# Performance work log

Hardware: AMD Instinct MI355X
Metric: run time of the kernel (lower is better)

Reference implementation:

```python
import jax, jax.numpy as jnp
import numpy as np

T = 0.07  # softmax temperature from __init__
N_QUEUES = 4


def _l2norm(x, axis):
    return x / jnp.maximum(jnp.linalg.norm(x, axis=axis, keepdims=True), 1e-12)


def setup_inputs() -> dict:
    key = jax.random.key(0)
    k1, k2, k3, k4, k5, k6 = jax.random.split(key, 6)
    N, D_in, dim, K = 512, 2048, 128, 65536
    im_q = jax.random.normal(k1, (N, D_in), dtype=jnp.float32)
    im_k = jax.random.normal(k2, (N, D_in), dtype=jnp.float32)
    W_q = jax.random.normal(k3, (D_in, dim), dtype=jnp.float32) * (1.0 / np.sqrt(D_in))
    W_k = jax.random.normal(k4, (D_in, dim), dtype=jnp.float32) * (1.0 / np.sqrt(D_in))
    queues = jax.random.normal(k5, (N_QUEUES, dim, K), dtype=jnp.float32)
    queues = _l2norm(queues, axis=1)  # normalize along feature dim, as in __init__
    label = jax.random.randint(k6, (N,), 0, 4, dtype=jnp.int32)
    return {"im_q": im_q, "im_k": im_k, "W_q": W_q, "W_k": W_k,
            "queues": queues, "label": label}


def reference(im_q, im_k, W_q, W_k, queues, label):
    # encoder_q / encoder_k abstracted as linear projections
    q = _l2norm(im_q @ W_q, axis=1)                      # [N, C]
    k = _l2norm(im_k @ W_k, axis=1)                      # [N, C] (no_grad in original)
    l_pos = jnp.einsum('nc,nc->n', q, k)[:, None]        # [N, 1]
    # per-sample queue routing: queue index = (label - 1) % 4
    route = jnp.mod(label - 1, N_QUEUES)                 # [N]
    onehot = jax.nn.one_hot(route, N_QUEUES, dtype=q.dtype)  # [N, G]
    # l_neg[n, k] = sum_c q[n, c] * queues[route[n], c, k], as grouped matmul
    l_neg = jnp.einsum('ngc,gck->nk', q[:, None, :] * onehot[:, :, None], queues)  # [N, K]
    logits = jnp.concatenate([l_pos, l_neg], axis=1) / T  # [N, 1+K]
    labels = jnp.zeros(logits.shape[0], dtype=jnp.int32)
    return logits, labels
```

## Files before the change

kernel.cpp:

```cpp
#include <hip/hip_runtime.h>

typedef short short8 __attribute__((ext_vector_type(8)));
typedef float floatx4 __attribute__((ext_vector_type(4)));

__device__ __forceinline__ unsigned short f2bf(float f) {
  unsigned u = __float_as_uint(f);
  u += 0x7FFFu + ((u >> 16) & 1u);
  return (unsigned short)(u >> 16);
}

__global__ __launch_bounds__(256) void proj_partial(
    const float* __restrict__ im_q, const float* __restrict__ im_k,
    const float* __restrict__ Wq, const float* __restrict__ Wk,
    float* __restrict__ part, int* __restrict__ cnt) {
  __shared__ float imS[32 * 260];
  const int t = threadIdx.x;
  if (blockIdx.x == 0 && blockIdx.y == 0 && blockIdx.z == 0 && t < 4) cnt[t] = 0;
  const int which = blockIdx.z;
  const float* __restrict__ im = which ? im_k : im_q;
  const float* __restrict__ W  = which ? Wk : Wq;
  const int d0 = blockIdx.x * 256;
  const int row0 = blockIdx.y * 32;
  {
    const int dd0 = (t & 63) * 4;
    const int rb = t >> 6;
#pragma unroll
    for (int p = 0; p < 8; ++p) {
      const int r = rb + p * 4;
      const float4 v = *(const float4*)(im + (size_t)(row0 + r) * 2048 + d0 + dd0);
      *(float4*)(imS + r * 260 + dd0) = v;
    }
  }
  __syncthreads();
  const int c4 = (t & 31) * 4;
  const int r4 = (t >> 5) * 4;
  float acc[4][4] = {};
  const float* __restrict__ Wp = W + (size_t)d0 * 128 + c4;
#pragma unroll 4
  for (int d = 0; d < 256; ++d) {
    const float4 w = *(const float4*)(Wp + (size_t)d * 128);
    float a[4];
#pragma unroll
    for (int rr = 0; rr < 4; ++rr) a[rr] = imS[(r4 + rr) * 260 + d];
#pragma unroll
    for (int rr = 0; rr < 4; ++rr) {
      acc[rr][0] += a[rr] * w.x;
      acc[rr][1] += a[rr] * w.y;
      acc[rr][2] += a[rr] * w.z;
      acc[rr][3] += a[rr] * w.w;
    }
  }
#pragma unroll
  for (int rr = 0; rr < 4; ++rr) {
    float4 v = make_float4(acc[rr][0], acc[rr][1], acc[rr][2], acc[rr][3]);
    *(float4*)(part + ((size_t)(which * 8 + blockIdx.x) * 512 + row0 + r4 + rr) * 128 + c4) = v;
  }
}

__global__ __launch_bounds__(128) void finalize(
    const float* __restrict__ part, const int* __restrict__ label,
    unsigned short* __restrict__ qbf, int* __restrict__ cnt,
    int* __restrict__ rows, float* __restrict__ out) {
  const int n = blockIdx.x, c = threadIdx.x;
  float qraw = 0.f, kraw = 0.f;
#pragma unroll
  for (int ch = 0; ch < 8; ++ch) {
    qraw += part[((size_t)ch * 512 + n) * 128 + c];
    kraw += part[((size_t)(8 + ch) * 512 + n) * 128 + c];
  }
  float sq = qraw * qraw, sk = kraw * kraw, dt = qraw * kraw;
#pragma unroll
  for (int off = 32; off > 0; off >>= 1) {
    sq += __shfl_down(sq, off, 64);
    sk += __shfl_down(sk, off, 64);
    dt += __shfl_down(dt, off, 64);
  }
  __shared__ float sh[3][2];
  const int lane = c & 63, wv = c >> 6;
  if (lane == 0) { sh[0][wv] = sq; sh[1][wv] = sk; sh[2][wv] = dt; }
  __syncthreads();
  const float tsq = sh[0][0] + sh[0][1];
  const float tsk = sh[1][0] + sh[1][1];
  const float tdt = sh[2][0] + sh[2][1];
  const float nq = fmaxf(sqrtf(tsq), 1e-12f);
  const float nk = fmaxf(sqrtf(tsk), 1e-12f);
  qbf[n * 128 + c] = f2bf(qraw / nq);
  if (c == 0) {
    out[(size_t)n * 65537] = tdt / (nq * nk) * (1.0f / 0.07f);
    ((int*)out)[(size_t)512 * 65537 + n] = 0;
    int g = ((label[n] - 1) % 4 + 4) % 4;
    int pos = atomicAdd(cnt + g, 1);
    rows[g * 512 + pos] = n;
  }
}

__global__ __launch_bounds__(256) void moco_lneg(
    const float* __restrict__ queues, const unsigned short* __restrict__ qbf,
    const int* __restrict__ cnt, const int* __restrict__ rows,
    float* __restrict__ out) {
  __shared__ unsigned short Bs[128 * 130];
  __shared__ unsigned short Qs[128 * 130];
  __shared__ int rowsS[128];
  const int g = blockIdx.y;
  const int Mg = cnt[g];
  if (Mg == 0) return;
  const int t = threadIdx.x;
  const int j0 = blockIdx.x * 128;
  {
    const int j = t & 127;
    const int cb = (t >> 7) * 64;
    const float* __restrict__ qb = queues + (size_t)g * 128 * 65536 + j0 + j;
#pragma unroll 8
    for (int p = 0; p < 32; ++p) {
      const int c = cb + p * 2;
      const float f0 = qb[(size_t)c * 65536];
      const float f1 = qb[(size_t)(c + 1) * 65536];
      const unsigned u = (unsigned)f2bf(f0) | ((unsigned)f2bf(f1) << 16);
      *(unsigned*)(Bs + j * 130 + c) = u;
    }
  }
  const int lane = t & 63, wave = t >> 6;
  const int qd = lane >> 4, l16 = lane & 15;
  const float invT = 1.0f / 0.07f;
  for (int chunk0 = 0; chunk0 < Mg; chunk0 += 128) {
    __syncthreads();
    const int valid = min(Mg - chunk0, 128);
    if (t < 128) rowsS[t] = (t < valid) ? rows[g * 512 + chunk0 + t] : 0;
    {
      const int m = t >> 1, half = (t & 1) * 64;
      if (m < valid) {
        const int rg = rows[g * 512 + chunk0 + m];
        const unsigned* __restrict__ src = (const unsigned*)(qbf + rg * 128 + half);
#pragma unroll
        for (int i = 0; i < 32; ++i)
          *(unsigned*)(Qs + m * 130 + half + i * 2) = src[i];
      } else {
#pragma unroll
        for (int i = 0; i < 32; ++i)
          *(unsigned*)(Qs + m * 130 + half + i * 2) = 0u;
      }
    }
    __syncthreads();
    floatx4 acc[8][2];
#pragma unroll
    for (int rb = 0; rb < 8; ++rb) {
      floatx4 z = {0.f, 0.f, 0.f, 0.f};
      acc[rb][0] = z; acc[rb][1] = z;
    }
#pragma unroll
    for (int kk = 0; kk < 4; ++kk) {
      const int k0 = kk * 32 + qd * 8;
      short8 bfrag[2];
#pragma unroll
      for (int s = 0; s < 2; ++s) {
        const unsigned* p = (const unsigned*)(Bs + ((wave * 2 + s) * 16 + l16) * 130 + k0);
        unsigned* d = (unsigned*)&bfrag[s];
        d[0] = p[0]; d[1] = p[1]; d[2] = p[2]; d[3] = p[3];
      }
#pragma unroll
      for (int rb = 0; rb < 8; ++rb) {
        const unsigned* p = (const unsigned*)(Qs + (rb * 16 + l16) * 130 + k0);
        short8 afrag;
        unsigned* d = (unsigned*)&afrag;
        d[0] = p[0]; d[1] = p[1]; d[2] = p[2]; d[3] = p[3];
        acc[rb][0] = __builtin_amdgcn_mfma_f32_16x16x32_bf16(afrag, bfrag[0], acc[rb][0], 0, 0, 0);
        acc[rb][1] = __builtin_amdgcn_mfma_f32_16x16x32_bf16(afrag, bfrag[1], acc[rb][1], 0, 0, 0);
      }
    }
#pragma unroll
    for (int rb = 0; rb < 8; ++rb) {
#pragma unroll
      for (int r = 0; r < 4; ++r) {
        const int ml = rb * 16 + qd * 4 + r;
        if (ml < valid) {
          const size_t base = (size_t)rowsS[ml] * 65537 + 1 + j0;
#pragma unroll
          for (int s = 0; s < 2; ++s)
            out[base + (wave * 2 + s) * 16 + l16] = acc[rb][s][r] * invT;
        }
      }
    }
  }
}

extern "C" void kernel_launch(void* const* d_in, const int* in_sizes, int n_in,
                              void* d_out, int out_size, void* d_ws, size_t ws_size,
                              hipStream_t stream) {
  const float* im_q   = (const float*)d_in[0];
  const float* im_k   = (const float*)d_in[1];
  const float* Wq     = (const float*)d_in[2];
  const float* Wk     = (const float*)d_in[3];
  const float* queues = (const float*)d_in[4];
  const int*   label  = (const int*)d_in[5];
  float* out = (float*)d_out;

  char* ws = (char*)d_ws;
  float* part = (float*)ws;
  unsigned short* qbf = (unsigned short*)(ws + (4u << 20));
  int* cnt  = (int*)(ws + (4u << 20) + (128u << 10));
  int* rows = cnt + 4;

  proj_partial<<<dim3(8, 16, 2), 256, 0, stream>>>(im_q, im_k, Wq, Wk, part, cnt);
  finalize<<<512, 128, 0, stream>>>(part, label, qbf, cnt, rows, out);
  moco_lneg<<<dim3(512, 4), 256, 0, stream>>>(queues, qbf, cnt, rows, out);
}
```

Baseline: 314.8 us.

## Read query fragments directly from global memory and shrink projection tiles

```diff
diff --git a/kernel.cpp b/kernel.cpp
--- a/kernel.cpp
+++ b/kernel.cpp
@@ -13,47 +13,43 @@
     const float* __restrict__ im_q, const float* __restrict__ im_k,
     const float* __restrict__ Wq, const float* __restrict__ Wk,
     float* __restrict__ part, int* __restrict__ cnt) {
-  __shared__ float imS[32 * 260];
+  __shared__ float imS[16 * 260];
   const int t = threadIdx.x;
   if (blockIdx.x == 0 && blockIdx.y == 0 && blockIdx.z == 0 && t < 4) cnt[t] = 0;
   const int which = blockIdx.z;
   const float* __restrict__ im = which ? im_k : im_q;
   const float* __restrict__ W  = which ? Wk : Wq;
   const int d0 = blockIdx.x * 256;
-  const int row0 = blockIdx.y * 32;
+  const int row0 = blockIdx.y * 16;
   {
     const int dd0 = (t & 63) * 4;
     const int rb = t >> 6;
 #pragma unroll
-    for (int p = 0; p < 8; ++p) {
-      const int r = rb + p * 4;
-      const float4 v = *(const float4*)(im + (size_t)(row0 + r) * 2048 + d0 + dd0);
-      *(float4*)(imS + r * 260 + dd0) = v;
+    for (int p = 0; p < 4; ++p) {
+      const int r = p * 4 + rb;
+      *(float4*)(imS + r * 260 + dd0) =
+          *(const float4*)(im + (size_t)(row0 + r) * 2048 + d0 + dd0);
     }
   }
   __syncthreads();
   const int c4 = (t & 31) * 4;
-  const int r4 = (t >> 5) * 4;
-  float acc[4][4] = {};
+  const int r2 = (t >> 5) * 2;
+  float acc[2][4] = {};
   const float* __restrict__ Wp = W + (size_t)d0 * 128 + c4;
-#pragma unroll 4
+#pragma unroll 8
   for (int d = 0; d < 256; ++d) {
     const float4 w = *(const float4*)(Wp + (size_t)d * 128);
-    float a[4];
-#pragma unroll
-    for (int rr = 0; rr < 4; ++rr) a[rr] = imS[(r4 + rr) * 260 + d];
-#pragma unroll
-    for (int rr = 0; rr < 4; ++rr) {
-      acc[rr][0] += a[rr] * w.x;
-      acc[rr][1] += a[rr] * w.y;
-      acc[rr][2] += a[rr] * w.z;
-      acc[rr][3] += a[rr] * w.w;
-    }
+    float a0 = imS[r2 * 260 + d];
+    float a1 = imS[(r2 + 1) * 260 + d];
+    acc[0][0] += a0 * w.x; acc[0][1] += a0 * w.y;
+    acc[0][2] += a0 * w.z; acc[0][3] += a0 * w.w;
+    acc[1][0] += a1 * w.x; acc[1][1] += a1 * w.y;
+    acc[1][2] += a1 * w.z; acc[1][3] += a1 * w.w;
   }
 #pragma unroll
-  for (int rr = 0; rr < 4; ++rr) {
+  for (int rr = 0; rr < 2; ++rr) {
     float4 v = make_float4(acc[rr][0], acc[rr][1], acc[rr][2], acc[rr][3]);
-    *(float4*)(part + ((size_t)(which * 8 + blockIdx.x) * 512 + row0 + r4 + rr) * 128 + c4) = v;
+    *(float4*)(part + ((size_t)(which * 8 + blockIdx.x) * 512 + row0 + r2 + rr) * 128 + c4) = v;
   }
 }
 
@@ -94,53 +90,42 @@
   }
 }
 
-__global__ __launch_bounds__(256) void moco_lneg(
+__global__ __launch_bounds__(256, 3) void moco_lneg(
     const float* __restrict__ queues, const unsigned short* __restrict__ qbf,
     const int* __restrict__ cnt, const int* __restrict__ rows,
     float* __restrict__ out) {
-  __shared__ unsigned short Bs[128 * 130];
-  __shared__ unsigned short Qs[128 * 130];
-  __shared__ int rowsS[128];
+  __shared__ __align__(16) unsigned short Bs[128 * 132];
+  __shared__ int rowsS[512];
   const int g = blockIdx.y;
   const int Mg = cnt[g];
   if (Mg == 0) return;
   const int t = threadIdx.x;
   const int j0 = blockIdx.x * 128;
+  rowsS[t] = rows[g * 512 + t];
+  rowsS[256 + t] = rows[g * 512 + 256 + t];
   {
     const int j = t & 127;
-    const int cb = (t >> 7) * 64;
+    const int ch = (t >> 7) * 4;
     const float* __restrict__ qb = queues + (size_t)g * 128 * 65536 + j0 + j;
-#pragma unroll 8
-    for (int p = 0; p < 32; ++p) {
-      const int c = cb + p * 2;
+#pragma unroll 4
+    for (int p = 0; p < 16; ++p) {
+      const int c = p * 8 + ch;
       const float f0 = qb[(size_t)c * 65536];
       const float f1 = qb[(size_t)(c + 1) * 65536];
-      const unsigned u = (unsigned)f2bf(f0) | ((unsigned)f2bf(f1) << 16);
-      *(unsigned*)(Bs + j * 130 + c) = u;
+      const float f2 = qb[(size_t)(c + 2) * 65536];
+      const float f3 = qb[(size_t)(c + 3) * 65536];
+      uint2 u;
+      u.x = (unsigned)f2bf(f0) | ((unsigned)f2bf(f1) << 16);
+      u.y = (unsigned)f2bf(f2) | ((unsigned)f2bf(f3) << 16);
+      *(uint2*)(Bs + j * 132 + c) = u;
     }
   }
+  __syncthreads();
   const int lane = t & 63, wave = t >> 6;
   const int qd = lane >> 4, l16 = lane & 15;
   const float invT = 1.0f / 0.07f;
   for (int chunk0 = 0; chunk0 < Mg; chunk0 += 128) {
-    __syncthreads();
     const int valid = min(Mg - chunk0, 128);
-    if (t < 128) rowsS[t] = (t < valid) ? rows[g * 512 + chunk0 + t] : 0;
-    {
-      const int m = t >> 1, half = (t & 1) * 64;
-      if (m < valid) {
-        const int rg = rows[g * 512 + chunk0 + m];
-        const unsigned* __restrict__ src = (const unsigned*)(qbf + rg * 128 + half);
-#pragma unroll
-        for (int i = 0; i < 32; ++i)
-          *(unsigned*)(Qs + m * 130 + half + i * 2) = src[i];
-      } else {
-#pragma unroll
-        for (int i = 0; i < 32; ++i)
-          *(unsigned*)(Qs + m * 130 + half + i * 2) = 0u;
-      }
-    }
-    __syncthreads();
     floatx4 acc[8][2];
 #pragma unroll
     for (int rb = 0; rb < 8; ++rb) {
@@ -153,16 +138,18 @@
       short8 bfrag[2];
 #pragma unroll
       for (int s = 0; s < 2; ++s) {
-        const unsigned* p = (const unsigned*)(Bs + ((wave * 2 + s) * 16 + l16) * 130 + k0);
-        unsigned* d = (unsigned*)&bfrag[s];
-        d[0] = p[0]; d[1] = p[1]; d[2] = p[2]; d[3] = p[3];
+        const uint2* p = (const uint2*)(Bs + ((wave * 2 + s) * 16 + l16) * 132 + k0);
+        uint2* d = (uint2*)&bfrag[s];
+        d[0] = p[0]; d[1] = p[1];
       }
 #pragma unroll
       for (int rb = 0; rb < 8; ++rb) {
-        const unsigned* p = (const unsigned*)(Qs + (rb * 16 + l16) * 130 + k0);
-        short8 afrag;
-        unsigned* d = (unsigned*)&afrag;
-        d[0] = p[0]; d[1] = p[1]; d[2] = p[2]; d[3] = p[3];
+        const int m = rb * 16 + l16;
+        short8 afrag = {};
+        if (m < valid) {
+          const int rg = rowsS[chunk0 + m];
+          *(uint4*)&afrag = *(const uint4*)(qbf + rg * 128 + k0);
+        }
         acc[rb][0] = __builtin_amdgcn_mfma_f32_16x16x32_bf16(afrag, bfrag[0], acc[rb][0], 0, 0, 0);
         acc[rb][1] = __builtin_amdgcn_mfma_f32_16x16x32_bf16(afrag, bfrag[1], acc[rb][1], 0, 0, 0);
       }
@@ -173,7 +160,7 @@
       for (int r = 0; r < 4; ++r) {
         const int ml = rb * 16 + qd * 4 + r;
         if (ml < valid) {
-          const size_t base = (size_t)rowsS[ml] * 65537 + 1 + j0;
+          const size_t base = (size_t)rowsS[chunk0 + ml] * 65537 + 1 + j0;
 #pragma unroll
           for (int s = 0; s < 2; ++s)
             out[base + (wave * 2 + s) * 16 + l16] = acc[rb][s][r] * invT;
@@ -200,7 +187,7 @@
   int* cnt  = (int*)(ws + (4u << 20) + (128u << 10));
   int* rows = cnt + 4;
 
-  proj_partial<<<dim3(8, 16, 2), 256, 0, stream>>>(im_q, im_k, Wq, Wk, part, cnt);
+  proj_partial<<<dim3(8, 32, 2), 256, 0, stream>>>(im_q, im_k, Wq, Wk, part, cnt);
   finalize<<<512, 128, 0, stream>>>(part, label, qbf, cnt, rows, out);
   moco_lneg<<<dim3(512, 4), 256, 0, stream>>>(queues, qbf, cnt, rows, out);
 }
```

Measured after the change: 324.4 us. 3.0% more time.
